# Performance work log

Hardware: AMD Instinct MI355X
Metric: run time of the kernel (lower is better)

The kernel has to match this reference:

```python
import jax, jax.numpy as jnp
import numpy as np

C = 256          # channels
K = 7            # involution kernel size
DIL = 1          # dilation
PAD = (K // 2) * DIL
RED = 4          # reduction ratio for kernel generation
GC = 16          # group channels
G = C // GC      # involution groups
EPS = 1e-5


def setup_inputs() -> dict:
    key = jax.random.key(0)
    ks = jax.random.split(key, 6)
    B, L = 8, 8192
    Cr = C // RED
    x = jax.random.normal(ks[0], (B, C, L), dtype=jnp.float32)
    w_reduce = jax.random.normal(ks[1], (Cr, C), dtype=jnp.float32) * 0.05
    w_span = jax.random.normal(ks[2], (G * K, Cr), dtype=jnp.float32) * 0.05
    prelu_a = jnp.asarray(0.25, dtype=jnp.float32)
    ln_gamma = jnp.ones((C,), dtype=jnp.float32)
    ln_beta = jnp.zeros((C,), dtype=jnp.float32)
    w_main = jax.random.normal(ks[3], (C, C), dtype=jnp.float32) * 0.05
    w_skip = jax.random.normal(ks[4], (C, C), dtype=jnp.float32) * 0.05
    return {"x": x, "w_reduce": w_reduce, "w_span": w_span,
            "prelu_a": prelu_a, "ln_gamma": ln_gamma, "ln_beta": ln_beta,
            "w_main": w_main, "w_skip": w_skip}


def reference(x, w_reduce, w_span, prelu_a, ln_gamma, ln_beta, w_main, w_skip):
    B, Cc, L = x.shape
    # --- Involution1D: dynamic per-position kernel generation (1x1 reduce + ReLU + 1x1 span) ---
    h = jax.nn.relu(jnp.einsum('rc,bcl->brl', w_reduce, x))              # (B, C/RED, L)
    ker = jnp.einsum('kr,brl->bkl', w_span, h).reshape(B, G, K, L)       # (B, G, K, L)
    # --- unfold x into sliding windows (stride 1, same padding) ---
    xp = jnp.pad(x, ((0, 0), (0, 0), (PAD, PAD)))
    xu = jnp.stack([jax.lax.dynamic_slice_in_dim(xp, k * DIL, L, axis=2)
                    for k in range(K)], axis=2)                           # (B, C, K, L)
    xu = xu.reshape(B, G, GC, K, L)
    out = jnp.einsum('bgkl,bgckl->bgcl', ker, xu).reshape(B, Cc, L)      # weighted sum over K
    # --- PReLU (single shared slope) ---
    out = jnp.where(out >= 0, out, prelu_a * out)
    # --- LayerNorm over channel dim (transpose->LN(C)->transpose) ---
    mu = jnp.mean(out, axis=1, keepdims=True)
    var = jnp.var(out, axis=1, keepdims=True)
    outn = (out - mu) * jax.lax.rsqrt(var + EPS)
    outn = outn * ln_gamma[None, :, None] + ln_beta[None, :, None]
    # --- pointwise convs + residual ---
    main_out = jnp.einsum('oc,bcl->bol', w_main, outn) + x
    skip = jnp.einsum('oc,bcl->bol', w_skip, outn)
    return main_out, skip
```

## Files before the change

kernel.cpp:

```cpp
#include <hip/hip_runtime.h>
#include <stdint.h>

#define C_DIM 256
#define L_DIM 8192
#define B_DIM 8
#define SKIP_OFF ((size_t)B_DIM * C_DIM * L_DIM)

using short8  = __attribute__((ext_vector_type(8))) short;
using floatx4 = __attribute__((ext_vector_type(4))) float;
typedef unsigned short ushort_t;

__device__ __forceinline__ ushort_t f2bf(float f) {
    union { float f; uint32_t u; } v; v.f = f;
    uint32_t u = v.u;
    return (ushort_t)((u + 0x7fff + ((u >> 16) & 1)) >> 16);
}
__device__ __forceinline__ float bf2f(ushort_t h) {
    union { uint32_t u; float f; } v; v.u = ((uint32_t)h) << 16;
    return v.f;
}

__device__ __forceinline__ int fragaddr(int l, int c) {
    return ((((l >> 4) * 8 + (c >> 5)) * 16 + (l & 15)) * 4 + ((c >> 3) & 3)) * 8 + (c & 7);
}

__global__ __launch_bounds__(256) void k0_prep(const float* __restrict__ wm,
                                               const float* __restrict__ wk,
                                               const float* __restrict__ wr,
                                               const float* __restrict__ wsp,
                                               ushort_t* __restrict__ wb,
                                               ushort_t* __restrict__ wrb,
                                               ushort_t* __restrict__ wsb) {
    int i = blockIdx.x * 256 + threadIdx.x;
    if (i < 65536) wb[i] = f2bf(wm[i]);
    else if (i < 131072) wb[i] = f2bf(wk[i - 65536]);
    else if (i < 147456) wrb[i - 131072] = f2bf(wr[i - 131072]);
    else if (i < 155648) {
        int j = i - 147456;
        int r = j >> 6, cc = j & 63;
        wsb[j] = (r < 112) ? f2bf(wsp[r * 64 + cc]) : (ushort_t)0;
    }
}

#define KST_STR 72
__global__ __launch_bounds__(256) void kf_front(const float* __restrict__ x,
                                                const ushort_t* __restrict__ wrb,
                                                const ushort_t* __restrict__ wsb,
                                                ushort_t* __restrict__ xbT,
                                                ushort_t* __restrict__ kb) {
    __shared__ ushort_t xsF[16384];
    __shared__ ushort_t hTF[4096];
    ushort_t* kst = xsF;

    int t = threadIdx.x;
    int b = blockIdx.x >> 7, l0 = (blockIdx.x & 127) * 64;
    const float* xb = x + (size_t)b * C_DIM * L_DIM;

    {
        int lo = (t & 15) * 4;
        int cbase = t >> 4;
#pragma unroll
        for (int j = 0; j < 16; ++j) {
            int c = cbase + j * 16;
            float4 v = *(const float4*)&xb[(size_t)c * L_DIM + l0 + lo];
            xsF[fragaddr(lo + 0, c)] = f2bf(v.x);
            xsF[fragaddr(lo + 1, c)] = f2bf(v.y);
            xsF[fragaddr(lo + 2, c)] = f2bf(v.z);
            xsF[fragaddr(lo + 3, c)] = f2bf(v.w);
        }
    }
    __syncthreads();

    {
        size_t base = ((size_t)b * L_DIM + l0) * C_DIM;
#pragma unroll
        for (int ii = 0; ii < 8; ++ii) {
            int i = t + ii * 256;
            int l = i >> 5, ch = i & 31;
            uint4 v = *(const uint4*)&xsF[fragaddr(l, ch * 8)];
            *(uint4*)&xbT[base + (size_t)l * C_DIM + ch * 8] = v;
        }
    }

    int w = t >> 6, lane = t & 63, lr = lane & 15, quad = lane >> 4;

    {
        short8 af[8];
#pragma unroll
        for (int s = 0; s < 8; ++s)
            af[s] = *(const short8*)&wrb[(w * 16 + lr) * 256 + s * 32 + quad * 8];
#pragma unroll
        for (int nt = 0; nt < 4; ++nt) {
            floatx4 acc = {0.f, 0.f, 0.f, 0.f};
#pragma unroll
            for (int s = 0; s < 8; ++s) {
                short8 bf = *(const short8*)&xsF[(((nt * 8 + s) * 16 + lr) * 4 + quad) * 8];
                acc = __builtin_amdgcn_mfma_f32_16x16x32_bf16(af[s], bf, acc, 0, 0, 0);
            }
            int r0 = w * 16 + quad * 4;
            int sK = r0 >> 5, quadK = (r0 >> 3) & 3, j0 = r0 & 7;
            ushort4 hv;
            hv.x = f2bf(fmaxf(acc[0], 0.f));
            hv.y = f2bf(fmaxf(acc[1], 0.f));
            hv.z = f2bf(fmaxf(acc[2], 0.f));
            hv.w = f2bf(fmaxf(acc[3], 0.f));
            *(ushort4*)&hTF[(((nt * 2 + sK) * 16 + lr) * 4 + quadK) * 8 + j0] = hv;
        }
    }
    __syncthreads();

#pragma unroll
    for (int mi = 0; mi < 2; ++mi) {
        int mt = w * 2 + mi;
        if (mt == 7) break;
        short8 aw[2];
#pragma unroll
        for (int s = 0; s < 2; ++s)
            aw[s] = *(const short8*)&wsb[(mt * 16 + lr) * 64 + s * 32 + quad * 8];
#pragma unroll
        for (int nt = 0; nt < 4; ++nt) {
            floatx4 acc = {0.f, 0.f, 0.f, 0.f};
#pragma unroll
            for (int s = 0; s < 2; ++s) {
                short8 bf = *(const short8*)&hTF[(((nt * 2 + s) * 16 + lr) * 4 + quad) * 8];
                acc = __builtin_amdgcn_mfma_f32_16x16x32_bf16(aw[s], bf, acc, 0, 0, 0);
            }
            int r0 = mt * 16 + quad * 4;
            int n  = nt * 16 + lr;
#pragma unroll
            for (int r = 0; r < 4; ++r)
                kst[(r0 + r) * KST_STR + n] = f2bf(acc[r]);
        }
    }
    __syncthreads();

#pragma unroll
    for (int ii = 0; ii < 4; ++ii) {
        int i = t + ii * 256;
        if (i < 896) {
            int r = i >> 3, ch = i & 7;
            uint4 v = *(const uint4*)&kst[r * KST_STR + ch * 8];
            *(uint4*)&kb[((size_t)b * 112 + r) * L_DIM + l0 + ch * 8] = v;
        }
    }
}

#define KS_STR 72
__global__ __launch_bounds__(256) void kg_back(const ushort_t* __restrict__ xbT,
                                               const ushort_t* __restrict__ kb,
                                               const ushort_t* __restrict__ wb,
                                               const float* __restrict__ x,
                                               const float* __restrict__ pa,
                                               const float* __restrict__ gamma,
                                               const float* __restrict__ beta,
                                               float* __restrict__ out) {
    __shared__ ushort_t ks[112 * KS_STR];
    __shared__ ushort_t xnF[16384];
    __shared__ float red1[256], red2[256];
    __shared__ float mean_s[64], rstd_s[64];

    int t = threadIdx.x;
    int b = blockIdx.x >> 7, l0 = (blockIdx.x & 127) * 64;

#pragma unroll
    for (int ii = 0; ii < 4; ++ii) {
        int i = t + ii * 256;
        if (i < 896) {
            int r = i >> 3, ch = i & 7;
            uint4 v = *(const uint4*)&kb[((size_t)b * 112 + r) * L_DIM + l0 + ch * 8];
            *(uint4*)&ks[r * KS_STR + ch * 8] = v;
        }
    }
    __syncthreads();

    int c = t, g = c >> 4;
    float aslope = pa[0], gam = gamma[c], bet = beta[c];
    const size_t xrow = (size_t)b * L_DIM * C_DIM;

    for (int hp = 0; hp < 2; ++hp) {
        int lbase = l0 + hp * 32;
        float xwin[38];
#pragma unroll
        for (int jj = 0; jj < 38; ++jj) {
            int l = lbase - 3 + jj;
            xwin[jj] = (l >= 0 && l < L_DIM) ? bf2f(xbT[xrow + (size_t)l * C_DIM + c]) : 0.f;
        }
        float acc[32];
#pragma unroll
        for (int j = 0; j < 32; ++j) acc[j] = 0.f;
#pragma unroll
        for (int k = 0; k < 7; ++k) {
            const ushort_t* krow = &ks[(g * 7 + k) * KS_STR + hp * 32];
#pragma unroll
            for (int ch = 0; ch < 4; ++ch) {
                ushort4 kp0 = *(const ushort4*)&krow[ch * 8];
                ushort4 kp1 = *(const ushort4*)&krow[ch * 8 + 4];
                float kv0 = bf2f(kp0.x), kv1 = bf2f(kp0.y), kv2 = bf2f(kp0.z), kv3 = bf2f(kp0.w);
                float kv4 = bf2f(kp1.x), kv5 = bf2f(kp1.y), kv6 = bf2f(kp1.z), kv7 = bf2f(kp1.w);
                acc[ch*8+0] = fmaf(kv0, xwin[ch*8 + 0 + k], acc[ch*8+0]);
                acc[ch*8+1] = fmaf(kv1, xwin[ch*8 + 1 + k], acc[ch*8+1]);
                acc[ch*8+2] = fmaf(kv2, xwin[ch*8 + 2 + k], acc[ch*8+2]);
                acc[ch*8+3] = fmaf(kv3, xwin[ch*8 + 3 + k], acc[ch*8+3]);
                acc[ch*8+4] = fmaf(kv4, xwin[ch*8 + 4 + k], acc[ch*8+4]);
                acc[ch*8+5] = fmaf(kv5, xwin[ch*8 + 5 + k], acc[ch*8+5]);
                acc[ch*8+6] = fmaf(kv6, xwin[ch*8 + 6 + k], acc[ch*8+6]);
                acc[ch*8+7] = fmaf(kv7, xwin[ch*8 + 7 + k], acc[ch*8+7]);
            }
        }
#pragma unroll
        for (int j = 0; j < 32; ++j) {
            acc[j] = acc[j] >= 0.f ? acc[j] : aslope * acc[j];
            xnF[fragaddr(hp * 32 + j, c)] = f2bf(acc[j]);
        }
        __syncthreads();
        {
            int lloc = hp * 32 + (t >> 3), seg = t & 7;
            float s1 = 0.f, s2 = 0.f;
#pragma unroll
            for (int q = 0; q < 4; ++q) {
                ushort4 v0 = *(const ushort4*)&xnF[fragaddr(lloc, seg * 32 + q * 8)];
                ushort4 v1 = *(const ushort4*)&xnF[fragaddr(lloc, seg * 32 + q * 8 + 4)];
                float f0 = bf2f(v0.x), f1 = bf2f(v0.y), f2v = bf2f(v0.z), f3 = bf2f(v0.w);
                float f4 = bf2f(v1.x), f5 = bf2f(v1.y), f6 = bf2f(v1.z), f7 = bf2f(v1.w);
                s1 += ((f0 + f1) + (f2v + f3)) + ((f4 + f5) + (f6 + f7));
                s2 += f0*f0 + f1*f1 + f2v*f2v + f3*f3 + f4*f4 + f5*f5 + f6*f6 + f7*f7;
            }
            red1[t] = s1; red2[t] = s2;
        }
        __syncthreads();
        if (t < 32) {
            float s1 = 0.f, s2 = 0.f;
#pragma unroll
            for (int i = 0; i < 8; ++i) { s1 += red1[t * 8 + i]; s2 += red2[t * 8 + i]; }
            float mu  = s1 * (1.f / 256.f);
            float var = s2 * (1.f / 256.f) - mu * mu;
            mean_s[hp * 32 + t] = mu;
            rstd_s[hp * 32 + t] = rsqrtf(var + 1e-5f);
        }
        __syncthreads();
#pragma unroll
        for (int j = 0; j < 32; ++j) {
            float v = (acc[j] - mean_s[hp * 32 + j]) * rstd_s[hp * 32 + j] * gam + bet;
            xnF[fragaddr(hp * 32 + j, c)] = f2bf(v);
        }
        __syncthreads();
    }

    int w = t >> 6, lane = t & 63, lr = lane & 15, quad = lane >> 4;
#pragma unroll
    for (int mi = 0; mi < 8; ++mi) {
        int mt = w * 8 + mi;
        const ushort_t* arow = wb + (size_t)(mt * 16 + lr) * 256 + quad * 8;
        short8 a[8];
#pragma unroll
        for (int s = 0; s < 8; ++s) a[s] = *(const short8*)(arow + s * 32);
#pragma unroll
        for (int nt = 0; nt < 4; ++nt) {
            floatx4 acc = {0.f, 0.f, 0.f, 0.f};
#pragma unroll
            for (int s = 0; s < 8; ++s) {
                short8 bfr = *(const short8*)&xnF[(((nt * 8 + s) * 16 + lr) * 4 + quad) * 8];
                acc = __builtin_amdgcn_mfma_f32_16x16x32_bf16(a[s], bfr, acc, 0, 0, 0);
            }
            int m = mt * 16 + quad * 4;
            int l = l0 + nt * 16 + lr;
            if (mt < 16) {
                size_t base = ((size_t)b * C_DIM + m) * L_DIM + l;
#pragma unroll
                for (int r = 0; r < 4; ++r)
                    out[base + (size_t)r * L_DIM] = acc[r] + x[base + (size_t)r * L_DIM];
            } else {
                size_t base = SKIP_OFF + ((size_t)b * C_DIM + (m - 256)) * L_DIM + l;
#pragma unroll
                for (int r = 0; r < 4; ++r)
                    out[base + (size_t)r * L_DIM] = acc[r];
            }
        }
    }
}

extern "C" void kernel_launch(void* const* d_in, const int* in_sizes, int n_in,
                              void* d_out, int out_size, void* d_ws, size_t ws_size,
                              hipStream_t stream) {
    const float* x     = (const float*)d_in[0];
    const float* w_red = (const float*)d_in[1];
    const float* w_spn = (const float*)d_in[2];
    const float* pa    = (const float*)d_in[3];
    const float* gam   = (const float*)d_in[4];
    const float* bet   = (const float*)d_in[5];
    const float* w_m   = (const float*)d_in[6];
    const float* w_s   = (const float*)d_in[7];
    float* out = (float*)d_out;

    char* ws = (char*)d_ws;
    ushort_t* wb  = (ushort_t*)(ws);
    ushort_t* wrb = (ushort_t*)(ws + 262144);
    ushort_t* wsb = (ushort_t*)(ws + 295040 - 128);
    ushort_t* xbT = (ushort_t*)(ws + 311296);
    ushort_t* kb  = (ushort_t*)(ws + 311296 + 33554432);

    k0_prep<<<608, 256, 0, stream>>>(w_m, w_s, w_red, w_spn, wb, wrb, wsb);
    kf_front<<<1024, 256, 0, stream>>>(x, wrb, wsb, xbT, kb);
    kg_back<<<1024, 256, 0, stream>>>(xbT, kb, wb, x, pa, gam, bet, out);
}
```

Baseline: 275.9 us.

## Fuse front and back kernels into one, dropping global bf16 intermediates

Merges the kernel-generation front kernel and the involution/LayerNorm/pointwise back kernel into a single kernel with 32-position tiles and 2048 blocks. It removes the transposed bf16 copy of x and the generated-kernel buffer that went through global memory, loading a 3-element halo per channel directly from x instead. The cost is that each block recomputes kernel generation only for its own tile, and the GEMM weight fragments are reloaded per smaller tile, which doubles weight traffic relative to output work.

```diff
diff --git a/kernel.cpp b/kernel.cpp
--- a/kernel.cpp
+++ b/kernel.cpp
@@ -42,45 +42,48 @@
     }
 }
 
-#define KST_STR 72
-__global__ __launch_bounds__(256) void kf_front(const float* __restrict__ x,
-                                                const ushort_t* __restrict__ wrb,
-                                                const ushort_t* __restrict__ wsb,
-                                                ushort_t* __restrict__ xbT,
-                                                ushort_t* __restrict__ kb) {
-    __shared__ ushort_t xsF[16384];
-    __shared__ ushort_t hTF[4096];
-    ushort_t* kst = xsF;
+#define KS_STR 40
+__global__ __launch_bounds__(256) void k_fused(const float* __restrict__ x,
+                                               const ushort_t* __restrict__ wrb,
+                                               const ushort_t* __restrict__ wsb,
+                                               const ushort_t* __restrict__ wb,
+                                               const float* __restrict__ pa,
+                                               const float* __restrict__ gamma,
+                                               const float* __restrict__ beta,
+                                               float* __restrict__ out) {
+    __shared__ __align__(16) ushort_t xsF[8192];
+    __shared__ __align__(16) ushort_t hTF[2048];
+    __shared__ __align__(16) ushort_t ks[112 * KS_STR];
 
     int t = threadIdx.x;
-    int b = blockIdx.x >> 7, l0 = (blockIdx.x & 127) * 64;
+    int b = blockIdx.x >> 8;
+    int l0 = (blockIdx.x & 255) * 32;
     const float* xb = x + (size_t)b * C_DIM * L_DIM;
 
+    int c = t;
+    float haloL[3], haloR[3];
+#pragma unroll
+    for (int j = 0; j < 3; ++j) {
+        int ll = l0 - 3 + j;
+        haloL[j] = (ll >= 0) ? xb[(size_t)c * L_DIM + ll] : 0.f;
+        int rr = l0 + 32 + j;
+        haloR[j] = (rr < L_DIM) ? xb[(size_t)c * L_DIM + rr] : 0.f;
+    }
+
     {
-        int lo = (t & 15) * 4;
-        int cbase = t >> 4;
-#pragma unroll
-        for (int j = 0; j < 16; ++j) {
-            int c = cbase + j * 16;
-            float4 v = *(const float4*)&xb[(size_t)c * L_DIM + l0 + lo];
-            xsF[fragaddr(lo + 0, c)] = f2bf(v.x);
-            xsF[fragaddr(lo + 1, c)] = f2bf(v.y);
-            xsF[fragaddr(lo + 2, c)] = f2bf(v.z);
-            xsF[fragaddr(lo + 3, c)] = f2bf(v.w);
-        }
-    }
-    __syncthreads();
-
-    {
-        size_t base = ((size_t)b * L_DIM + l0) * C_DIM;
-#pragma unroll
-        for (int ii = 0; ii < 8; ++ii) {
-            int i = t + ii * 256;
-            int l = i >> 5, ch = i & 31;
-            uint4 v = *(const uint4*)&xsF[fragaddr(l, ch * 8)];
-            *(uint4*)&xbT[base + (size_t)l * C_DIM + ch * 8] = v;
-        }
-    }
+        int lo = (t & 7) * 4;
+        int cb = t >> 3;
+#pragma unroll
+        for (int j = 0; j < 8; ++j) {
+            int cc = cb + j * 32;
+            float4 v = *(const float4*)&xb[(size_t)cc * L_DIM + l0 + lo];
+            xsF[fragaddr(lo + 0, cc)] = f2bf(v.x);
+            xsF[fragaddr(lo + 1, cc)] = f2bf(v.y);
+            xsF[fragaddr(lo + 2, cc)] = f2bf(v.z);
+            xsF[fragaddr(lo + 3, cc)] = f2bf(v.w);
+        }
+    }
+    __syncthreads();
 
     int w = t >> 6, lane = t & 63, lr = lane & 15, quad = lane >> 4;
 
@@ -90,21 +93,21 @@
         for (int s = 0; s < 8; ++s)
             af[s] = *(const short8*)&wrb[(w * 16 + lr) * 256 + s * 32 + quad * 8];
 #pragma unroll
-        for (int nt = 0; nt < 4; ++nt) {
-            floatx4 acc = {0.f, 0.f, 0.f, 0.f};
+        for (int nt = 0; nt < 2; ++nt) {
+            floatx4 a4 = {0.f, 0.f, 0.f, 0.f};
 #pragma unroll
             for (int s = 0; s < 8; ++s) {
                 short8 bf = *(const short8*)&xsF[(((nt * 8 + s) * 16 + lr) * 4 + quad) * 8];
-                acc = __builtin_amdgcn_mfma_f32_16x16x32_bf16(af[s], bf, acc, 0, 0, 0);
+                a4 = __builtin_amdgcn_mfma_f32_16x16x32_bf16(af[s], bf, a4, 0, 0, 0);
             }
             int r0 = w * 16 + quad * 4;
-            int sK = r0 >> 5, quadK = (r0 >> 3) & 3, j0 = r0 & 7;
+            int sK = r0 >> 5, qK = (r0 >> 3) & 3, j0 = r0 & 7;
             ushort4 hv;
-            hv.x = f2bf(fmaxf(acc[0], 0.f));
-            hv.y = f2bf(fmaxf(acc[1], 0.f));
-            hv.z = f2bf(fmaxf(acc[2], 0.f));
-            hv.w = f2bf(fmaxf(acc[3], 0.f));
-            *(ushort4*)&hTF[(((nt * 2 + sK) * 16 + lr) * 4 + quadK) * 8 + j0] = hv;
+            hv.x = f2bf(fmaxf(a4[0], 0.f));
+            hv.y = f2bf(fmaxf(a4[1], 0.f));
+            hv.z = f2bf(fmaxf(a4[2], 0.f));
+            hv.w = f2bf(fmaxf(a4[3], 0.f));
+            *(ushort4*)&hTF[(((nt * 2 + sK) * 16 + lr) * 4 + qK) * 8 + j0] = hv;
         }
     }
     __syncthreads();
@@ -118,135 +121,97 @@
         for (int s = 0; s < 2; ++s)
             aw[s] = *(const short8*)&wsb[(mt * 16 + lr) * 64 + s * 32 + quad * 8];
 #pragma unroll
-        for (int nt = 0; nt < 4; ++nt) {
-            floatx4 acc = {0.f, 0.f, 0.f, 0.f};
+        for (int nt = 0; nt < 2; ++nt) {
+            floatx4 a4 = {0.f, 0.f, 0.f, 0.f};
 #pragma unroll
             for (int s = 0; s < 2; ++s) {
                 short8 bf = *(const short8*)&hTF[(((nt * 2 + s) * 16 + lr) * 4 + quad) * 8];
-                acc = __builtin_amdgcn_mfma_f32_16x16x32_bf16(aw[s], bf, acc, 0, 0, 0);
+                a4 = __builtin_amdgcn_mfma_f32_16x16x32_bf16(aw[s], bf, a4, 0, 0, 0);
             }
             int r0 = mt * 16 + quad * 4;
             int n  = nt * 16 + lr;
 #pragma unroll
             for (int r = 0; r < 4; ++r)
-                kst[(r0 + r) * KST_STR + n] = f2bf(acc[r]);
-        }
-    }
-    __syncthreads();
-
-#pragma unroll
-    for (int ii = 0; ii < 4; ++ii) {
-        int i = t + ii * 256;
-        if (i < 896) {
-            int r = i >> 3, ch = i & 7;
-            uint4 v = *(const uint4*)&kst[r * KST_STR + ch * 8];
-            *(uint4*)&kb[((size_t)b * 112 + r) * L_DIM + l0 + ch * 8] = v;
-        }
-    }
-}
-
-#define KS_STR 72
-__global__ __launch_bounds__(256) void kg_back(const ushort_t* __restrict__ xbT,
-                                               const ushort_t* __restrict__ kb,
-                                               const ushort_t* __restrict__ wb,
-                                               const float* __restrict__ x,
-                                               const float* __restrict__ pa,
-                                               const float* __restrict__ gamma,
-                                               const float* __restrict__ beta,
-                                               float* __restrict__ out) {
-    __shared__ ushort_t ks[112 * KS_STR];
-    __shared__ ushort_t xnF[16384];
-    __shared__ float red1[256], red2[256];
-    __shared__ float mean_s[64], rstd_s[64];
-
-    int t = threadIdx.x;
-    int b = blockIdx.x >> 7, l0 = (blockIdx.x & 127) * 64;
-
-#pragma unroll
-    for (int ii = 0; ii < 4; ++ii) {
-        int i = t + ii * 256;
-        if (i < 896) {
-            int r = i >> 3, ch = i & 7;
-            uint4 v = *(const uint4*)&kb[((size_t)b * 112 + r) * L_DIM + l0 + ch * 8];
-            *(uint4*)&ks[r * KS_STR + ch * 8] = v;
-        }
-    }
-    __syncthreads();
-
-    int c = t, g = c >> 4;
+                ks[(r0 + r) * KS_STR + n] = f2bf(a4[r]);
+        }
+    }
+    __syncthreads();
+
+    int g = c >> 4;
     float aslope = pa[0], gam = gamma[c], bet = beta[c];
-    const size_t xrow = (size_t)b * L_DIM * C_DIM;
-
-    for (int hp = 0; hp < 2; ++hp) {
-        int lbase = l0 + hp * 32;
-        float xwin[38];
-#pragma unroll
-        for (int jj = 0; jj < 38; ++jj) {
-            int l = lbase - 3 + jj;
-            xwin[jj] = (l >= 0 && l < L_DIM) ? bf2f(xbT[xrow + (size_t)l * C_DIM + c]) : 0.f;
-        }
-        float acc[32];
-#pragma unroll
-        for (int j = 0; j < 32; ++j) acc[j] = 0.f;
-#pragma unroll
-        for (int k = 0; k < 7; ++k) {
-            const ushort_t* krow = &ks[(g * 7 + k) * KS_STR + hp * 32];
-#pragma unroll
-            for (int ch = 0; ch < 4; ++ch) {
-                ushort4 kp0 = *(const ushort4*)&krow[ch * 8];
-                ushort4 kp1 = *(const ushort4*)&krow[ch * 8 + 4];
-                float kv0 = bf2f(kp0.x), kv1 = bf2f(kp0.y), kv2 = bf2f(kp0.z), kv3 = bf2f(kp0.w);
-                float kv4 = bf2f(kp1.x), kv5 = bf2f(kp1.y), kv6 = bf2f(kp1.z), kv7 = bf2f(kp1.w);
-                acc[ch*8+0] = fmaf(kv0, xwin[ch*8 + 0 + k], acc[ch*8+0]);
-                acc[ch*8+1] = fmaf(kv1, xwin[ch*8 + 1 + k], acc[ch*8+1]);
-                acc[ch*8+2] = fmaf(kv2, xwin[ch*8 + 2 + k], acc[ch*8+2]);
-                acc[ch*8+3] = fmaf(kv3, xwin[ch*8 + 3 + k], acc[ch*8+3]);
-                acc[ch*8+4] = fmaf(kv4, xwin[ch*8 + 4 + k], acc[ch*8+4]);
-                acc[ch*8+5] = fmaf(kv5, xwin[ch*8 + 5 + k], acc[ch*8+5]);
-                acc[ch*8+6] = fmaf(kv6, xwin[ch*8 + 6 + k], acc[ch*8+6]);
-                acc[ch*8+7] = fmaf(kv7, xwin[ch*8 + 7 + k], acc[ch*8+7]);
-            }
-        }
-#pragma unroll
-        for (int j = 0; j < 32; ++j) {
-            acc[j] = acc[j] >= 0.f ? acc[j] : aslope * acc[j];
-            xnF[fragaddr(hp * 32 + j, c)] = f2bf(acc[j]);
-        }
-        __syncthreads();
-        {
-            int lloc = hp * 32 + (t >> 3), seg = t & 7;
-            float s1 = 0.f, s2 = 0.f;
-#pragma unroll
-            for (int q = 0; q < 4; ++q) {
-                ushort4 v0 = *(const ushort4*)&xnF[fragaddr(lloc, seg * 32 + q * 8)];
-                ushort4 v1 = *(const ushort4*)&xnF[fragaddr(lloc, seg * 32 + q * 8 + 4)];
-                float f0 = bf2f(v0.x), f1 = bf2f(v0.y), f2v = bf2f(v0.z), f3 = bf2f(v0.w);
-                float f4 = bf2f(v1.x), f5 = bf2f(v1.y), f6 = bf2f(v1.z), f7 = bf2f(v1.w);
-                s1 += ((f0 + f1) + (f2v + f3)) + ((f4 + f5) + (f6 + f7));
-                s2 += f0*f0 + f1*f1 + f2v*f2v + f3*f3 + f4*f4 + f5*f5 + f6*f6 + f7*f7;
-            }
-            red1[t] = s1; red2[t] = s2;
-        }
-        __syncthreads();
-        if (t < 32) {
-            float s1 = 0.f, s2 = 0.f;
-#pragma unroll
-            for (int i = 0; i < 8; ++i) { s1 += red1[t * 8 + i]; s2 += red2[t * 8 + i]; }
-            float mu  = s1 * (1.f / 256.f);
-            float var = s2 * (1.f / 256.f) - mu * mu;
-            mean_s[hp * 32 + t] = mu;
-            rstd_s[hp * 32 + t] = rsqrtf(var + 1e-5f);
-        }
-        __syncthreads();
-#pragma unroll
-        for (int j = 0; j < 32; ++j) {
-            float v = (acc[j] - mean_s[hp * 32 + j]) * rstd_s[hp * 32 + j] * gam + bet;
-            xnF[fragaddr(hp * 32 + j, c)] = f2bf(v);
-        }
-        __syncthreads();
-    }
-
-    int w = t >> 6, lane = t & 63, lr = lane & 15, quad = lane >> 4;
+    float xwin[38];
+    xwin[0] = haloL[0]; xwin[1] = haloL[1]; xwin[2] = haloL[2];
+#pragma unroll
+    for (int j = 0; j < 32; ++j) xwin[3 + j] = bf2f(xsF[fragaddr(j, c)]);
+    xwin[35] = haloR[0]; xwin[36] = haloR[1]; xwin[37] = haloR[2];
+
+    float acc[32];
+#pragma unroll
+    for (int j = 0; j < 32; ++j) acc[j] = 0.f;
+#pragma unroll
+    for (int k = 0; k < 7; ++k) {
+        const ushort_t* krow = &ks[(g * 7 + k) * KS_STR];
+#pragma unroll
+        for (int ch = 0; ch < 4; ++ch) {
+            ushort4 kp0 = *(const ushort4*)&krow[ch * 8];
+            ushort4 kp1 = *(const ushort4*)&krow[ch * 8 + 4];
+            float kv0 = bf2f(kp0.x), kv1 = bf2f(kp0.y), kv2 = bf2f(kp0.z), kv3 = bf2f(kp0.w);
+            float kv4 = bf2f(kp1.x), kv5 = bf2f(kp1.y), kv6 = bf2f(kp1.z), kv7 = bf2f(kp1.w);
+            acc[ch*8+0] = fmaf(kv0, xwin[ch*8 + 0 + k], acc[ch*8+0]);
+            acc[ch*8+1] = fmaf(kv1, xwin[ch*8 + 1 + k], acc[ch*8+1]);
+            acc[ch*8+2] = fmaf(kv2, xwin[ch*8 + 2 + k], acc[ch*8+2]);
+            acc[ch*8+3] = fmaf(kv3, xwin[ch*8 + 3 + k], acc[ch*8+3]);
+            acc[ch*8+4] = fmaf(kv4, xwin[ch*8 + 4 + k], acc[ch*8+4]);
+            acc[ch*8+5] = fmaf(kv5, xwin[ch*8 + 5 + k], acc[ch*8+5]);
+            acc[ch*8+6] = fmaf(kv6, xwin[ch*8 + 6 + k], acc[ch*8+6]);
+            acc[ch*8+7] = fmaf(kv7, xwin[ch*8 + 7 + k], acc[ch*8+7]);
+        }
+    }
+    __syncthreads();
+
+#pragma unroll
+    for (int j = 0; j < 32; ++j) {
+        acc[j] = acc[j] >= 0.f ? acc[j] : aslope * acc[j];
+        xsF[fragaddr(j, c)] = f2bf(acc[j]);
+    }
+    __syncthreads();
+
+    float* red1   = (float*)hTF;
+    float* red2   = red1 + 256;
+    float* mean_s = red2 + 256;
+    float* rstd_s = mean_s + 32;
+    {
+        int lloc = t >> 3, seg = t & 7;
+        float s1 = 0.f, s2 = 0.f;
+#pragma unroll
+        for (int q = 0; q < 4; ++q) {
+            ushort4 v0 = *(const ushort4*)&xsF[fragaddr(lloc, seg * 32 + q * 8)];
+            ushort4 v1 = *(const ushort4*)&xsF[fragaddr(lloc, seg * 32 + q * 8 + 4)];
+            float f0 = bf2f(v0.x), f1 = bf2f(v0.y), f2v = bf2f(v0.z), f3 = bf2f(v0.w);
+            float f4 = bf2f(v1.x), f5 = bf2f(v1.y), f6 = bf2f(v1.z), f7 = bf2f(v1.w);
+            s1 += ((f0 + f1) + (f2v + f3)) + ((f4 + f5) + (f6 + f7));
+            s2 += f0*f0 + f1*f1 + f2v*f2v + f3*f3 + f4*f4 + f5*f5 + f6*f6 + f7*f7;
+        }
+        red1[t] = s1; red2[t] = s2;
+    }
+    __syncthreads();
+    if (t < 32) {
+        float s1 = 0.f, s2 = 0.f;
+#pragma unroll
+        for (int i = 0; i < 8; ++i) { s1 += red1[t * 8 + i]; s2 += red2[t * 8 + i]; }
+        float mu  = s1 * (1.f / 256.f);
+        float var = s2 * (1.f / 256.f) - mu * mu;
+        mean_s[t] = mu;
+        rstd_s[t] = rsqrtf(var + 1e-5f);
+    }
+    __syncthreads();
+#pragma unroll
+    for (int j = 0; j < 32; ++j) {
+        float v = (acc[j] - mean_s[j]) * rstd_s[j] * gam + bet;
+        xsF[fragaddr(j, c)] = f2bf(v);
+    }
+    __syncthreads();
+
 #pragma unroll
     for (int mi = 0; mi < 8; ++mi) {
         int mt = w * 8 + mi;
@@ -255,12 +220,12 @@
 #pragma unroll
         for (int s = 0; s < 8; ++s) a[s] = *(const short8*)(arow + s * 32);
 #pragma unroll
-        for (int nt = 0; nt < 4; ++nt) {
-            floatx4 acc = {0.f, 0.f, 0.f, 0.f};
+        for (int nt = 0; nt < 2; ++nt) {
+            floatx4 a4 = {0.f, 0.f, 0.f, 0.f};
 #pragma unroll
             for (int s = 0; s < 8; ++s) {
-                short8 bfr = *(const short8*)&xnF[(((nt * 8 + s) * 16 + lr) * 4 + quad) * 8];
-                acc = __builtin_amdgcn_mfma_f32_16x16x32_bf16(a[s], bfr, acc, 0, 0, 0);
+                short8 bfr = *(const short8*)&xsF[(((nt * 8 + s) * 16 + lr) * 4 + quad) * 8];
+                a4 = __builtin_amdgcn_mfma_f32_16x16x32_bf16(a[s], bfr, a4, 0, 0, 0);
             }
             int m = mt * 16 + quad * 4;
             int l = l0 + nt * 16 + lr;
@@ -268,12 +233,12 @@
                 size_t base = ((size_t)b * C_DIM + m) * L_DIM + l;
 #pragma unroll
                 for (int r = 0; r < 4; ++r)
-                    out[base + (size_t)r * L_DIM] = acc[r] + x[base + (size_t)r * L_DIM];
+                    out[base + (size_t)r * L_DIM] = a4[r] + x[base + (size_t)r * L_DIM];
             } else {
                 size_t base = SKIP_OFF + ((size_t)b * C_DIM + (m - 256)) * L_DIM + l;
 #pragma unroll
                 for (int r = 0; r < 4; ++r)
-                    out[base + (size_t)r * L_DIM] = acc[r];
+                    out[base + (size_t)r * L_DIM] = a4[r];
             }
         }
     }
@@ -295,11 +260,8 @@
     char* ws = (char*)d_ws;
     ushort_t* wb  = (ushort_t*)(ws);
     ushort_t* wrb = (ushort_t*)(ws + 262144);
-    ushort_t* wsb = (ushort_t*)(ws + 295040 - 128);
-    ushort_t* xbT = (ushort_t*)(ws + 311296);
-    ushort_t* kb  = (ushort_t*)(ws + 311296 + 33554432);
+    ushort_t* wsb = (ushort_t*)(ws + 294912);
 
     k0_prep<<<608, 256, 0, stream>>>(w_m, w_s, w_red, w_spn, wb, wrb, wsb);
-    kf_front<<<1024, 256, 0, stream>>>(x, wrb, wsb, xbT, kb);
-    kg_back<<<1024, 256, 0, stream>>>(xbT, kb, wb, x, pa, gam, bet, out);
-}
+    k_fused<<<2048, 256, 0, stream>>>(x, wrb, wsb, wb, pa, gam, bet, out);
+}
```

After: 279.1 us. Within noise of the previous version (+1.1%).
